# Kernel optimization log

Hardware: AMD Instinct MI355X
Metric: run time of the kernel (lower is better)

The kernel has to match this reference:

```python
import jax, jax.numpy as jnp
import numpy as np

N_QUBITS = 8
N_PAIRS = 4
PAIRS = [(2 * p, 2 * p + 1) for p in range(N_PAIRS)]
STRENGTH = 0.8
DIM = 2 ** N_QUBITS


def _apply_1q_full(st, G, q):
    # st: (2,)*n complex64 state, G: [2,2] gate on qubit q (qubit 0 = most significant)
    out = jnp.tensordot(G, st, axes=([1], [q]))
    return jnp.moveaxis(out, 0, q)


def _apply_ctrl_full(st, G, c, t):
    # controlled-G: apply G on target axis t only where control axis c == 1
    s0 = jnp.take(st, 0, axis=c)
    s1 = jnp.take(st, 1, axis=c)
    t2 = t if t < c else t - 1
    s1 = jnp.moveaxis(jnp.tensordot(G, s1, axes=([1], [t2])), 0, t2)
    return jnp.stack([s0, s1], axis=c)


def _entangled_base():
    # |0...0> -> H on q1, partial CNOT (controlled-RX(pi*strength)) on (q1,q2) per pair
    st = jnp.zeros((2,) * N_QUBITS, jnp.complex64).at[(0,) * N_QUBITS].set(1.0)
    H = jnp.array([[1.0, 1.0], [1.0, -1.0]], jnp.complex64) / np.float32(np.sqrt(2.0))
    th = np.float32(np.pi * STRENGTH)
    c, s = np.float32(np.cos(th / 2)), np.float32(np.sin(th / 2))
    RX = jnp.array([[c, -1j * s], [-1j * s, c]], jnp.complex64)
    for q1, q2 in PAIRS:
        st = _apply_1q_full(st, H, q1)
        st = _apply_ctrl_full(st, RX, q1, q2)
    return st.reshape(-1)


def _rx(theta):
    # RX(theta) = [[cos t/2, -i sin t/2], [-i sin t/2, cos t/2]], batched over theta shape
    cz = jnp.cos(0.5 * theta).astype(jnp.complex64)
    sz = (-1j) * jnp.sin(0.5 * theta).astype(jnp.complex64)
    return jnp.stack([jnp.stack([cz, sz], -1), jnpp_stack_fix(sz, cz)], -2) if False else jnp.stack([jnp.stack([cz, sz], -1), jnp.stack([sz, cz], -1)], -2)


def _rz(theta):
    ph = (0.5j) * theta.astype(jnp.complex64)
    e0, e1 = jnp.exp(-ph), jnp.exp(ph)
    z = jnp.zeros_like(e0)
    return jnp.stack([jnp.stack([e0, z], -1), jnp.stack([z, e1], -1)], -2)


def _quantum_scores(k_states):
    # k_states: [B,S,2*n_qubits] -> expected pair-agreement score [B,S]
    B, S, _ = k_states.shape
    k = k_states.reshape(B, S, N_QUBITS, 2)
    eye = jnp.eye(2, dtype=jnp.complex64)
    st = jnp.broadcast_to(_entangled_base(), (B, S, DIM))  # fresh entangled register per (b,j)
    for q in range(N_QUBITS):
        th_x, th_z = k[:, :, q, 0], k[:, :, q, 1]
        Gx = jnp.where((th_x > 0)[..., None, None], _rx(th_x), eye)
        Gz = jnp.where((th_z > 0)[..., None, None], _rz(th_z), eye)
        G = jnp.einsum('bsij,bsjk->bsik', Gz, Gx)  # RX applied first, then RZ
        L = 2 ** q
        R = DIM // (2 * L)
        stv = st.reshape(B, S, L, 2, R)
        st = jnp.einsum('bsij,bsljr->bslir', G, stv).reshape(B, S, DIM)
    probs = (st.real ** 2 + st.imag ** 2).reshape((B, S) + (2,) * N_QUBITS)
    score = jnp.zeros((B, S), probs.dtype)
    for q1, q2 in PAIRS:
        axes = tuple(2 + a for a in range(N_QUBITS) if a not in (q1, q2))
        marg = probs.sum(axis=axes)  # [B,S,2,2] joint marginal of the pair
        score = score + marg[..., 0, 0] + marg[..., 1, 1]  # P(measure equal)
    return score / N_PAIRS


def reference(query, key, value, Wq, bq, Wk, bk, Wv, bv, Wo, bo):
    q_states = query @ Wq + bq  # computed as in original forward (unused by scores)
    k_states = key @ Wk + bk    # [B,S,2*n_qubits]
    v_states = value @ Wv + bv  # [B,S,d_model]
    B, S, _ = k_states.shape
    score = _quantum_scores(k_states)  # [B,S]; deterministic expected agreement
    # original loop makes score[b,i,j] independent of i under independent per-(b,i,j) sims
    attn = jnp.broadcast_to(score[:, None, :], (B, S, S))
    w = jax.nn.softmax(attn, axis=-1)
    out = jnp.einsum('bij,bjd->bid', w, v_states)
    return out @ Wo + bo


def setup_inputs() -> dict:
    rng = jax.random.key(0)
    ks = jax.random.split(rng, 8)
    B, S, D = 8, 2048, 512
    nq2 = 2 * N_QUBITS
    f = jax.random.normal
    return {
        'query': f(ks[0], (B, S, D), jnp.float32),
        'key': f(ks[1], (B, S, D), jnp.float32),
        'value': f(ks[2], (B, S, D), jnp.float32),
        'Wq': f(ks[3], (D, nq2), jnp.float32) * 0.05,
        'bq': jnp.zeros((nq2,), jnp.float32),
        'Wk': f(ks[4], (D, nq2), jnp.float32) * 0.05,
        'bk': jnp.zeros((nq2,), jnp.float32),
        'Wv': f(ks[5], (D, D), jnp.float32) * 0.05,
        'bv': jnp.zeros((D,), jnp.float32),
        'Wo': f(ks[6], (D, D), jnp.float32) * 0.05,
        'bo': jnp.zeros((D,), jnp.float32),
    }
```

## Files before the change

kernel.cpp:

```cpp
#include <hip/hip_runtime.h>
#include <math.h>

#define DEV __device__ __forceinline__

struct C2 { float x, y; };
DEV C2 cmul(C2 a, C2 b){ return {a.x*b.x - a.y*b.y, a.x*b.y + a.y*b.x}; }
DEV C2 cadd(C2 a, C2 b){ return {a.x+b.x, a.y+b.y}; }
DEV C2 cscale(C2 a, float s){ return {a.x*s, a.y*s}; }
DEV C2 cnegi(C2 a){ return {a.y, -a.x}; }

__global__ __launch_bounds__(512, 4) void k_score_wsum(const float* __restrict__ key,
                                                       const float* __restrict__ Wk,
                                                       const float* __restrict__ bk,
                                                       const float* __restrict__ value,
                                                       float* __restrict__ partial,
                                                       float* __restrict__ partialw)
{
    const int c = blockIdx.x;
    const int b = blockIdx.y;
    const int t = threadIdx.x;
    const int lane = t & 63;
    const int wv   = t >> 6;
    const int base = b * 2048 + c * 32;
    const int r0   = base + wv * 4;

    __shared__ float  kslds[32][16];
    __shared__ float4 red[8][128];
    __shared__ float  wsums[8];

    float4 wk[8][4];
    #pragma unroll
    for (int jj = 0; jj < 4; ++jj) {
        const float4* w0 = (const float4*)(Wk + (4 * lane + jj) * 16);
        const float4* w1 = (const float4*)(Wk + (256 + 4 * lane + jj) * 16);
        #pragma unroll
        for (int q = 0; q < 4; ++q) { wk[jj][q] = w0[q]; wk[4 + jj][q] = w1[q]; }
    }
    const float bkr = bk[lane & 15];
    const float c0 = 0.30901699437494745f;
    const float s0 = 0.9510565162951535f;

    const float4* kp = (const float4*)(key + (size_t)r0 * 512);
    float4 a0 = kp[lane],       a1 = kp[64 + lane];
    float4 b0 = kp[128 + lane], b1 = kp[192 + lane];
    #pragma unroll
    for (int i = 0; i < 4; i += 2) {
        float4 na0, na1, nb0, nb1;
        if (i < 2) {
            na0 = kp[(i + 2) * 128 + lane]; na1 = kp[(i + 2) * 128 + 64 + lane];
            nb0 = kp[(i + 3) * 128 + lane]; nb1 = kp[(i + 3) * 128 + 64 + lane];
        }
        float eA[8] = {a0.x, a0.y, a0.z, a0.w, a1.x, a1.y, a1.z, a1.w};
        float eB[8] = {b0.x, b0.y, b0.z, b0.w, b1.x, b1.y, b1.z, b1.w};
        float accA[16], accB[16];
        #pragma unroll
        for (int k = 0; k < 16; ++k) { accA[k] = 0.f; accB[k] = 0.f; }
        #pragma unroll
        for (int jr = 0; jr < 8; ++jr) {
            #pragma unroll
            for (int q = 0; q < 4; ++q) {
                accA[4*q+0] = fmaf(eA[jr], wk[jr][q].x, accA[4*q+0]);
                accA[4*q+1] = fmaf(eA[jr], wk[jr][q].y, accA[4*q+1]);
                accA[4*q+2] = fmaf(eA[jr], wk[jr][q].z, accA[4*q+2]);
                accA[4*q+3] = fmaf(eA[jr], wk[jr][q].w, accA[4*q+3]);
                accB[4*q+0] = fmaf(eB[jr], wk[jr][q].x, accB[4*q+0]);
                accB[4*q+1] = fmaf(eB[jr], wk[jr][q].y, accB[4*q+1]);
                accB[4*q+2] = fmaf(eB[jr], wk[jr][q].z, accB[4*q+2]);
                accB[4*q+3] = fmaf(eB[jr], wk[jr][q].w, accB[4*q+3]);
            }
        }
        #pragma unroll
        for (int s = 0; s < 4; ++s) {
            const int m = 1 << s;
            const int bbit = (lane >> s) & 1;
            #pragma unroll
            for (int jj = 0; jj < (16 >> (s + 1)); ++jj) {
                float sA = bbit ? accA[2*jj] : accA[2*jj+1];
                float kA = bbit ? accA[2*jj+1] : accA[2*jj];
                accA[jj] = kA + __shfl_xor(sA, m);
                float sB = bbit ? accB[2*jj] : accB[2*jj+1];
                float kB = bbit ? accB[2*jj+1] : accB[2*jj];
                accB[jj] = kB + __shfl_xor(sB, m);
            }
        }
        float ksA = accA[0];
        ksA += __shfl_xor(ksA, 16); ksA += __shfl_xor(ksA, 32); ksA += bkr;
        float ksB = accB[0];
        ksB += __shfl_xor(ksB, 16); ksB += __shfl_xor(ksB, 32); ksB += bkr;
        if (lane < 16) {
            kslds[wv * 4 + i][lane]     = ksA;
            kslds[wv * 4 + i + 1][lane] = ksB;
        }
        if (i < 2) { a0 = na0; a1 = na1; b0 = nb0; b1 = nb1; }
    }

    const float4* vp = (const float4*)(value + (size_t)r0 * 512);
    float4 vreg[8];
    #pragma unroll
    for (int j = 0; j < 4; ++j) {
        vreg[2*j]   = vp[j * 128 + lane];
        vreg[2*j+1] = vp[j * 128 + 64 + lane];
    }

    const int p  = (lane >> 2) & 3;
    const int jr = lane & 3;
    float4 kv = *(const float4*)&kslds[wv * 4 + jr][4 * p];
    float ax = kv.x, az = kv.y, bx = kv.z, bz = kv.w;
    float cxa = 1.f, sxa = 0.f; if (ax > 0.f){ sxa = __sinf(0.5f*ax); cxa = __cosf(0.5f*ax); }
    float cpa = 1.f, spa = 0.f; if (az > 0.f){ spa = __sinf(0.5f*az); cpa = __cosf(0.5f*az); }
    float cxb = 1.f, sxb = 0.f; if (bx > 0.f){ sxb = __sinf(0.5f*bx); cxb = __cosf(0.5f*bx); }
    float cpb = 1.f, spb = 0.f; if (bz > 0.f){ spb = __sinf(0.5f*bz); cpb = __cosf(0.5f*bz); }
    C2 A00{cpa*cxa, -spa*cxa}, A01{-spa*sxa, -cpa*sxa};
    C2 A10{spa*sxa, -cpa*sxa}, A11{ cpa*cxa,  spa*cxa};
    C2 B00{cpb*cxb, -spb*cxb}, B01{-spb*sxb, -cpb*sxb};
    C2 B10{spb*sxb, -cpb*sxb}, B11{ cpb*cxb,  spb*cxb};
    C2 u = cadd(cmul(B00, cadd(A00, cscale(A01, c0))),
                cscale(cnegi(cmul(A01, B01)), s0));
    C2 v = cadd(cmul(B10, cadd(A10, cscale(A11, c0))),
                cscale(cnegi(cmul(A11, B11)), s0));
    float ps = u.x*u.x + u.y*u.y + v.x*v.x + v.y*v.y;
    ps += __shfl_xor(ps, 4);
    ps += __shfl_xor(ps, 8);
    float w_all = __expf(ps * 0.125f);

    float sw = w_all;
    sw += __shfl_xor(sw, 1); sw += __shfl_xor(sw, 2);
    if (lane == 0) wsums[wv] = sw;

    float4 aA = {0.f,0.f,0.f,0.f}, aB = {0.f,0.f,0.f,0.f};
    #pragma unroll
    for (int j = 0; j < 4; ++j) {
        float wj = __shfl(w_all, j);
        float4 v0 = vreg[2*j], v1 = vreg[2*j+1];
        aA.x = fmaf(wj, v0.x, aA.x); aA.y = fmaf(wj, v0.y, aA.y);
        aA.z = fmaf(wj, v0.z, aA.z); aA.w = fmaf(wj, v0.w, aA.w);
        aB.x = fmaf(wj, v1.x, aB.x); aB.y = fmaf(wj, v1.y, aB.y);
        aB.z = fmaf(wj, v1.z, aB.z); aB.w = fmaf(wj, v1.w, aB.w);
    }
    red[wv][lane] = aA;
    red[wv][64 + lane] = aB;
    __syncthreads();
    if (t < 128) {
        float4 q0 = red[0][t], q1 = red[1][t], q2 = red[2][t], q3 = red[3][t];
        float4 q4 = red[4][t], q5 = red[5][t], q6 = red[6][t], q7 = red[7][t];
        float4 o = { q0.x+q1.x+q2.x+q3.x+q4.x+q5.x+q6.x+q7.x,
                     q0.y+q1.y+q2.y+q3.y+q4.y+q5.y+q6.y+q7.y,
                     q0.z+q1.z+q2.z+q3.z+q4.z+q5.z+q6.z+q7.z,
                     q0.w+q1.w+q2.w+q3.w+q4.w+q5.w+q6.w+q7.w };
        ((float4*)partial)[((size_t)b * 64 + c) * 128 + t] = o;
    }
    if (t == 0)
        partialw[b * 64 + c] = wsums[0] + wsums[1] + wsums[2] + wsums[3]
                             + wsums[4] + wsums[5] + wsums[6] + wsums[7];
}

__global__ __launch_bounds__(256) void k_ctx(const float* __restrict__ partial,
                                             const float* __restrict__ partialw,
                                             const float* __restrict__ Wv,
                                             const float* __restrict__ bv,
                                             float* __restrict__ ctx)
{
    int dt = blockIdx.x, b = blockIdx.y, t = threadIdx.x;
    __shared__ float4 red4[2][128];
    __shared__ float  vb[512];
    __shared__ float  red[256];
    __shared__ float  invS;

    if (t < 64) {
        float s = partialw[b * 64 + t];
        s += __shfl_xor(s, 1);  s += __shfl_xor(s, 2);
        s += __shfl_xor(s, 4);  s += __shfl_xor(s, 8);
        s += __shfl_xor(s, 16); s += __shfl_xor(s, 32);
        if (t == 0) invS = 1.f / s;
    }
    const int col4 = t & 127, cg = t >> 7;
    const float4* pp4 = (const float4*)partial
                      + ((size_t)b * 64 + cg * 32) * 128 + col4;
    float4 a = {0.f, 0.f, 0.f, 0.f};
    #pragma unroll 8
    for (int cc = 0; cc < 32; ++cc) {
        float4 v = pp4[(size_t)cc * 128];
        a.x += v.x; a.y += v.y; a.z += v.z; a.w += v.w;
    }
    red4[cg][col4] = a;
    __syncthreads();
    if (t < 128) {
        float4 q0 = red4[0][t], q1 = red4[1][t];
        float is = invS;
        vb[4*t+0] = (q0.x + q1.x) * is;
        vb[4*t+1] = (q0.y + q1.y) * is;
        vb[4*t+2] = (q0.z + q1.z) * is;
        vb[4*t+3] = (q0.w + q1.w) * is;
    }
    __syncthreads();

    int dl = t & 63, q = t >> 6;
    int d = dt * 64 + dl;
    const float* x  = vb + q * 128;
    const float* Wc = Wv + (size_t)(q * 128) * 512 + d;
    float acc = 0.f;
    #pragma unroll 8
    for (int e = 0; e < 128; ++e) acc = fmaf(x[e], Wc[(size_t)e * 512], acc);
    red[t] = acc; __syncthreads();
    if (t < 64)
        ctx[b * 512 + dt * 64 + t] = red[t] + red[t+64] + red[t+128] + red[t+192]
                                   + bv[dt * 64 + t];
}

__global__ __launch_bounds__(256) void k_frow(const float* __restrict__ ctx,
                                              const float* __restrict__ Wo,
                                              const float* __restrict__ bo,
                                              float* __restrict__ frow)
{
    int dt = blockIdx.x, b = blockIdx.y, t = threadIdx.x;
    __shared__ float xs[512];
    __shared__ float red[256];

    xs[t]       = ctx[b * 512 + t];
    xs[t + 256] = ctx[b * 512 + 256 + t];
    __syncthreads();

    int dl = t & 63, q = t >> 6;
    int d = dt * 64 + dl;
    const float* x  = xs + q * 128;
    const float* Wc = Wo + (size_t)(q * 128) * 512 + d;
    float acc = 0.f;
    #pragma unroll 8
    for (int e = 0; e < 128; ++e) acc = fmaf(x[e], Wc[(size_t)e * 512], acc);
    red[t] = acc; __syncthreads();
    if (t < 64)
        frow[b * 512 + dt * 64 + t] = red[t] + red[t+64] + red[t+128] + red[t+192]
                                    + bo[dt * 64 + t];
}

__global__ __launch_bounds__(256) void k_bcast(const float* __restrict__ frow,
                                               float* __restrict__ out)
{
    int s = blockIdx.x, b = blockIdx.y, t = threadIdx.x;
    const int col4 = t & 127, h = t >> 7;
    float4 val = ((const float4*)frow)[b * 128 + col4];
    float4* o4 = (float4*)out
               + ((size_t)b * 2048 + s * 32 + h * 16) * 128 + col4;
    #pragma unroll
    for (int r = 0; r < 16; ++r) o4[(size_t)r * 128] = val;
}

extern "C" void kernel_launch(void* const* d_in, const int* in_sizes, int n_in,
                              void* d_out, int out_size, void* d_ws, size_t ws_size,
                              hipStream_t stream) {
    const float* key   = (const float*)d_in[1];
    const float* value = (const float*)d_in[2];
    const float* Wk    = (const float*)d_in[5];
    const float* bk    = (const float*)d_in[6];
    const float* Wv    = (const float*)d_in[7];
    const float* bv    = (const float*)d_in[8];
    const float* Wo    = (const float*)d_in[9];
    const float* bo    = (const float*)d_in[10];
    float* out = (float*)d_out;
    float* ws  = (float*)d_ws;

    float* partial  = ws;
    float* partialw = ws + 262144;
    float* ctx      = ws + 262656;
    float* frow     = ws + 266752;

    k_score_wsum<<<dim3(64, 8), 512, 0, stream>>>(key, Wk, bk, value,
                                                  partial, partialw);
    k_ctx <<<dim3(8, 8),  256, 0, stream>>>(partial, partialw, Wv, bv, ctx);
    k_frow<<<dim3(8, 8),  256, 0, stream>>>(ctx, Wo, bo, frow);
    k_bcast<<<dim3(64, 8), 256, 0, stream>>>(frow, out);
}
```

Baseline: 199.4 us.

## Split key projection across wave pairs to halve Wk register footprint

Each pair of waves now splits the 512-wide key dot product: each wave holds half of Wk in registers (4x4 float4 instead of 8x4) and processes 8 rows over its half of the columns. The partial sums are written to two LDS planes and combined, with the bias added, after a new block barrier. The aim is lower register pressure, and with it better occupancy or less spilling, in the memory-bound score kernel. The cost is an extra __syncthreads and more LDS traffic, and score evaluation now spans 8 rows per wave with adjusted shuffles.

Measured after the change: 170.2 us. 1.17x faster.

```diff
diff --git a/kernel.cpp b/kernel.cpp
--- a/kernel.cpp
+++ b/kernel.cpp
@@ -21,52 +21,43 @@
     const int t = threadIdx.x;
     const int lane = t & 63;
     const int wv   = t >> 6;
+    const int h    = wv & 1;
+    const int pr   = wv >> 1;
     const int base = b * 2048 + c * 32;
-    const int r0   = base + wv * 4;
-
-    __shared__ float  kslds[32][16];
+    const int wrow0 = pr * 8;
+
+    __shared__ float  kslds[2][32][16];
     __shared__ float4 red[8][128];
-    __shared__ float  wsums[8];
-
-    float4 wk[8][4];
+    __shared__ float  wsums[4];
+
+    float4 wk[4][4];
     #pragma unroll
     for (int jj = 0; jj < 4; ++jj) {
-        const float4* w0 = (const float4*)(Wk + (4 * lane + jj) * 16);
-        const float4* w1 = (const float4*)(Wk + (256 + 4 * lane + jj) * 16);
-        #pragma unroll
-        for (int q = 0; q < 4; ++q) { wk[jj][q] = w0[q]; wk[4 + jj][q] = w1[q]; }
-    }
-    const float bkr = bk[lane & 15];
+        const float4* w0 = (const float4*)(Wk + (h * 256 + 4 * lane + jj) * 16);
+        #pragma unroll
+        for (int q = 0; q < 4; ++q) wk[jj][q] = w0[q];
+    }
     const float c0 = 0.30901699437494745f;
     const float s0 = 0.9510565162951535f;
 
-    const float4* kp = (const float4*)(key + (size_t)r0 * 512);
-    float4 a0 = kp[lane],       a1 = kp[64 + lane];
-    float4 b0 = kp[128 + lane], b1 = kp[192 + lane];
-    #pragma unroll
-    for (int i = 0; i < 4; i += 2) {
-        float4 na0, na1, nb0, nb1;
-        if (i < 2) {
-            na0 = kp[(i + 2) * 128 + lane]; na1 = kp[(i + 2) * 128 + 64 + lane];
-            nb0 = kp[(i + 3) * 128 + lane]; nb1 = kp[(i + 3) * 128 + 64 + lane];
-        }
-        float eA[8] = {a0.x, a0.y, a0.z, a0.w, a1.x, a1.y, a1.z, a1.w};
-        float eB[8] = {b0.x, b0.y, b0.z, b0.w, b1.x, b1.y, b1.z, b1.w};
-        float accA[16], accB[16];
-        #pragma unroll
-        for (int k = 0; k < 16; ++k) { accA[k] = 0.f; accB[k] = 0.f; }
-        #pragma unroll
-        for (int jr = 0; jr < 8; ++jr) {
+    const float4* kp = (const float4*)(key + (size_t)(base + wrow0) * 512);
+    float4 cur = kp[h * 64 + lane];
+    #pragma unroll
+    for (int j = 0; j < 8; ++j) {
+        float4 nx;
+        if (j < 7) nx = kp[(j + 1) * 128 + h * 64 + lane];
+        float el[4] = {cur.x, cur.y, cur.z, cur.w};
+        float acc[16];
+        #pragma unroll
+        for (int k = 0; k < 16; ++k) acc[k] = 0.f;
+        #pragma unroll
+        for (int jj = 0; jj < 4; ++jj) {
             #pragma unroll
             for (int q = 0; q < 4; ++q) {
-                accA[4*q+0] = fmaf(eA[jr], wk[jr][q].x, accA[4*q+0]);
-                accA[4*q+1] = fmaf(eA[jr], wk[jr][q].y, accA[4*q+1]);
-                accA[4*q+2] = fmaf(eA[jr], wk[jr][q].z, accA[4*q+2]);
-                accA[4*q+3] = fmaf(eA[jr], wk[jr][q].w, accA[4*q+3]);
-                accB[4*q+0] = fmaf(eB[jr], wk[jr][q].x, accB[4*q+0]);
-                accB[4*q+1] = fmaf(eB[jr], wk[jr][q].y, accB[4*q+1]);
-                accB[4*q+2] = fmaf(eB[jr], wk[jr][q].z, accB[4*q+2]);
-                accB[4*q+3] = fmaf(eB[jr], wk[jr][q].w, accB[4*q+3]);
+                acc[4*q+0] = fmaf(el[jj], wk[jj][q].x, acc[4*q+0]);
+                acc[4*q+1] = fmaf(el[jj], wk[jj][q].y, acc[4*q+1]);
+                acc[4*q+2] = fmaf(el[jj], wk[jj][q].z, acc[4*q+2]);
+                acc[4*q+3] = fmaf(el[jj], wk[jj][q].w, acc[4*q+3]);
             }
         }
         #pragma unroll
@@ -75,37 +66,35 @@
             const int bbit = (lane >> s) & 1;
             #pragma unroll
             for (int jj = 0; jj < (16 >> (s + 1)); ++jj) {
-                float sA = bbit ? accA[2*jj] : accA[2*jj+1];
-                float kA = bbit ? accA[2*jj+1] : accA[2*jj];
-                accA[jj] = kA + __shfl_xor(sA, m);
-                float sB = bbit ? accB[2*jj] : accB[2*jj+1];
-                float kB = bbit ? accB[2*jj+1] : accB[2*jj];
-                accB[jj] = kB + __shfl_xor(sB, m);
+                float send = bbit ? acc[2*jj] : acc[2*jj+1];
+                float keep = bbit ? acc[2*jj+1] : acc[2*jj];
+                acc[jj] = keep + __shfl_xor(send, m);
             }
         }
-        float ksA = accA[0];
-        ksA += __shfl_xor(ksA, 16); ksA += __shfl_xor(ksA, 32); ksA += bkr;
-        float ksB = accB[0];
-        ksB += __shfl_xor(ksB, 16); ksB += __shfl_xor(ksB, 32); ksB += bkr;
-        if (lane < 16) {
-            kslds[wv * 4 + i][lane]     = ksA;
-            kslds[wv * 4 + i + 1][lane] = ksB;
-        }
-        if (i < 2) { a0 = na0; a1 = na1; b0 = nb0; b1 = nb1; }
-    }
-
-    const float4* vp = (const float4*)(value + (size_t)r0 * 512);
+        float ks = acc[0];
+        ks += __shfl_xor(ks, 16);
+        ks += __shfl_xor(ks, 32);
+        if (lane < 16) kslds[h][wrow0 + j][lane] = ks;
+        cur = nx;
+    }
+
+    const int vrow0 = wrow0 + h * 4;
+    const float4* vp = (const float4*)(value + (size_t)(base + vrow0) * 512);
     float4 vreg[8];
     #pragma unroll
     for (int j = 0; j < 4; ++j) {
         vreg[2*j]   = vp[j * 128 + lane];
         vreg[2*j+1] = vp[j * 128 + 64 + lane];
     }
-
-    const int p  = (lane >> 2) & 3;
-    const int jr = lane & 3;
-    float4 kv = *(const float4*)&kslds[wv * 4 + jr][4 * p];
-    float ax = kv.x, az = kv.y, bx = kv.z, bz = kv.w;
+    __syncthreads();
+
+    const int p  = (lane >> 3) & 3;
+    const int jr = lane & 7;
+    float4 k0 = *(const float4*)&kslds[0][wrow0 + jr][4 * p];
+    float4 k1 = *(const float4*)&kslds[1][wrow0 + jr][4 * p];
+    float4 bk4 = ((const float4*)bk)[p];
+    float ax = k0.x + k1.x + bk4.x, az = k0.y + k1.y + bk4.y;
+    float bx = k0.z + k1.z + bk4.z, bz = k0.w + k1.w + bk4.w;
     float cxa = 1.f, sxa = 0.f; if (ax > 0.f){ sxa = __sinf(0.5f*ax); cxa = __cosf(0.5f*ax); }
     float cpa = 1.f, spa = 0.f; if (az > 0.f){ spa = __sinf(0.5f*az); cpa = __cosf(0.5f*az); }
     float cxb = 1.f, sxb = 0.f; if (bx > 0.f){ sxb = __sinf(0.5f*bx); cxb = __cosf(0.5f*bx); }
@@ -119,18 +108,20 @@
     C2 v = cadd(cmul(B10, cadd(A10, cscale(A11, c0))),
                 cscale(cnegi(cmul(A11, B11)), s0));
     float ps = u.x*u.x + u.y*u.y + v.x*v.x + v.y*v.y;
-    ps += __shfl_xor(ps, 4);
     ps += __shfl_xor(ps, 8);
+    ps += __shfl_xor(ps, 16);
     float w_all = __expf(ps * 0.125f);
 
-    float sw = w_all;
-    sw += __shfl_xor(sw, 1); sw += __shfl_xor(sw, 2);
-    if (lane == 0) wsums[wv] = sw;
+    if (h == 0) {
+        float sw = w_all;
+        sw += __shfl_xor(sw, 1); sw += __shfl_xor(sw, 2); sw += __shfl_xor(sw, 4);
+        if (lane == 0) wsums[pr] = sw;
+    }
 
     float4 aA = {0.f,0.f,0.f,0.f}, aB = {0.f,0.f,0.f,0.f};
     #pragma unroll
     for (int j = 0; j < 4; ++j) {
-        float wj = __shfl(w_all, j);
+        float wj = __shfl(w_all, h * 4 + j);
         float4 v0 = vreg[2*j], v1 = vreg[2*j+1];
         aA.x = fmaf(wj, v0.x, aA.x); aA.y = fmaf(wj, v0.y, aA.y);
         aA.z = fmaf(wj, v0.z, aA.z); aA.w = fmaf(wj, v0.w, aA.w);
@@ -150,8 +141,7 @@
         ((float4*)partial)[((size_t)b * 64 + c) * 128 + t] = o;
     }
     if (t == 0)
-        partialw[b * 64 + c] = wsums[0] + wsums[1] + wsums[2] + wsums[3]
-                             + wsums[4] + wsums[5] + wsums[6] + wsums[7];
+        partialw[b * 64 + c] = wsums[0] + wsums[1] + wsums[2] + wsums[3];
 }
 
 __global__ __launch_bounds__(256) void k_ctx(const float* __restrict__ partial,
```
